# Kernel tuning notes

Measured on AMD Instinct MI355X. Metric: run time of the kernel, lower is better.

## Reference

```python
import jax, jax.numpy as jnp
import numpy as np

D = 1024  # input_size
NORM = 1.0 / np.sqrt(D)


def setup_inputs() -> dict:
    key = jax.random.key(0)
    k_x, k_q, k_k, k_v = jax.random.split(key, 4)
    B, S = 4, 2048
    scale = 1.0 / np.sqrt(D)  # init ~ nn.Linear default magnitude
    return {
        "inputs": jax.random.normal(k_x, (B, S, D), dtype=jnp.float32),
        "Wq": jax.random.uniform(k_q, (D, D), jnp.float32, -scale, scale),
        "Wk": jax.random.uniform(k_k, (D, D), jnp.float32, -scale, scale),
        "Wv": jax.random.uniform(k_v, (D, D), jnp.float32, -scale, scale),
    }


def reference(inputs, Wq, Wk, Wv):
    # nn.Linear(x) = x @ W.T (no bias)
    Q = jnp.einsum("bsd,ed->bse", inputs, Wq)
    K = jnp.einsum("bsd,ed->bse", inputs, Wk)
    V = jnp.einsum("bsd,ed->bse", inputs, Wv)
    attn = jnp.einsum("bqe,bke->bqk", Q, K) * NORM  # [B,S,S]
    attn = jax.nn.softmax(attn, axis=2)
    return jnp.einsum("bqk,bke->bqe", attn, V)
```

## Files before the change

kernel.cpp:

```cpp
#include <hip/hip_runtime.h>

typedef __bf16 bf16_t;
typedef __bf16 bf16x8 __attribute__((ext_vector_type(8)));
typedef __bf16 bf16x4 __attribute__((ext_vector_type(4)));
typedef float  floatx4 __attribute__((ext_vector_type(4)));

__device__ __forceinline__ void gload_lds16(const bf16_t* g, bf16_t* l) {
    __builtin_amdgcn_global_load_lds(
        (const __attribute__((address_space(1))) void*)g,
        (__attribute__((address_space(3))) void*)l,
        16, 0, 0);
}

template <int MODE, int BKT, typename OutT>
__global__ __launch_bounds__(256) void gemm_nt(
    const bf16_t* __restrict__ A, int lda, size_t batchA,
    const bf16_t* __restrict__ B, int ldb, size_t batchB,
    OutT* __restrict__ C, int ldc, size_t batchC,
    bf16_t* __restrict__ C2, int ldc2,
    float* __restrict__ rowsums, int batchR,
    int K, float scale)
{
    constexpr int CH  = BKT / 8;
    constexpr int RPS = 2048 / BKT;
    constexpr int NSHOT = 128 / RPS;

    __shared__ bf16_t sA[128 * BKT];
    __shared__ bf16_t sB[128 * BKT];

    A += (size_t)blockIdx.z * batchA;
    B += (size_t)blockIdx.z * batchB;

    const int tid  = threadIdx.x;
    const int wid  = tid >> 6;
    const int lane = tid & 63;

    const int bm = blockIdx.x * 128;
    const int bn = blockIdx.y * 128;

    const int rr  = tid / CH;
    const int kc8 = (((tid & (CH - 1)) ^ (rr & (CH - 1))) << 3);

    const int wy = (wid >> 1) * 64;
    const int wx = (wid & 1) * 64;
    const int lr = lane & 15;

    floatx4 acc[4][4] = {};

    const bf16_t* pa = A + (size_t)(bm + rr) * lda + kc8;
    const bf16_t* pb = B + (size_t)(bn + rr) * ldb + kc8;
    bf16_t* la = &sA[wid * 512];
    bf16_t* lb = &sB[wid * 512];

    for (int k0 = 0; k0 < K; k0 += BKT) {
        #pragma unroll
        for (int c = 0; c < NSHOT; ++c) {
            gload_lds16(pa + (size_t)(c * RPS) * lda + k0, la + c * 2048);
            gload_lds16(pb + (size_t)(c * RPS) * ldb + k0, lb + c * 2048);
        }
        __syncthreads();

        #pragma unroll
        for (int kk = 0; kk < BKT / 32; ++kk) {
            const int cch = (kk << 2) + (lane >> 4);
            bf16x8 af[4], bq[4];
            #pragma unroll
            for (int i = 0; i < 4; ++i) {
                int r = wy + i * 16 + lr;
                af[i] = *(const bf16x8*)&sA[r * BKT + ((cch ^ (r & (CH - 1))) << 3)];
            }
            #pragma unroll
            for (int j = 0; j < 4; ++j) {
                int r = wx + j * 16 + lr;
                bq[j] = *(const bf16x8*)&sB[r * BKT + ((cch ^ (r & (CH - 1))) << 3)];
            }
            #pragma unroll
            for (int i = 0; i < 4; ++i)
                #pragma unroll
                for (int j = 0; j < 4; ++j)
                    acc[i][j] = __builtin_amdgcn_mfma_f32_16x16x32_bf16(
                        bq[j], af[i], acc[i][j], 0, 0, 0);
        }
        __syncthreads();
    }

    const int cfix = lane & 15;
    const int creg = (lane >> 4) << 2;

    if constexpr (MODE == 1) {
        if (blockIdx.z == 2) {
            #pragma unroll
            for (int i = 0; i < 4; ++i) {
                int mg = bm + wy + i * 16 + cfix;
                #pragma unroll
                for (int j = 0; j < 4; ++j) {
                    int ng = bn + wx + j * 16 + creg;
                    #pragma unroll
                    for (int r = 0; r < 4; ++r)
                        C2[(size_t)(ng + r) * ldc2 + mg] = (bf16_t)acc[i][j][r];
                }
            }
            return;
        }
        OutT* Cz = C + (size_t)blockIdx.z * batchC;
        #pragma unroll
        for (int i = 0; i < 4; ++i) {
            size_t row = (size_t)(bm + wy + i * 16 + cfix);
            #pragma unroll
            for (int j = 0; j < 4; ++j) {
                int col = bn + wx + j * 16 + creg;
                bf16x4 v;
                #pragma unroll
                for (int r = 0; r < 4; ++r) v[r] = (bf16_t)acc[i][j][r];
                *(bf16x4*)&Cz[row * (size_t)ldc + col] = v;
            }
        }
    } else if constexpr (MODE == 2) {
        OutT* Cz = C + (size_t)blockIdx.z * batchC;
        float* sums = rowsums + (size_t)blockIdx.z * batchR;
        float rs[4] = {0.f, 0.f, 0.f, 0.f};
        #pragma unroll
        for (int i = 0; i < 4; ++i) {
            size_t row = (size_t)(bm + wy + i * 16 + cfix);
            #pragma unroll
            for (int j = 0; j < 4; ++j) {
                int col = bn + wx + j * 16 + creg;
                bf16x4 v;
                #pragma unroll
                for (int r = 0; r < 4; ++r) {
                    v[r] = (bf16_t)__expf(acc[i][j][r] * scale);
                    rs[i] += (float)v[r];
                }
                *(bf16x4*)&Cz[row * (size_t)ldc + col] = v;
            }
        }
        #pragma unroll
        for (int i = 0; i < 4; ++i) {
            rs[i] += __shfl_xor(rs[i], 16);
            rs[i] += __shfl_xor(rs[i], 32);
        }
        if (lane < 16) {
            #pragma unroll
            for (int i = 0; i < 4; ++i)
                atomicAdd(&sums[bm + wy + i * 16 + lane], rs[i]);
        }
    } else {
        OutT* Cz = C + (size_t)blockIdx.z * batchC;
        const float* sums = rowsums + (size_t)blockIdx.z * batchR;
        #pragma unroll
        for (int i = 0; i < 4; ++i) {
            int rloc = bm + wy + i * 16 + cfix;
            float rinv = 1.0f / sums[rloc];
            size_t row = (size_t)rloc;
            #pragma unroll
            for (int j = 0; j < 4; ++j) {
                int col = bn + wx + j * 16 + creg;
                floatx4 v;
                #pragma unroll
                for (int r = 0; r < 4; ++r) v[r] = acc[i][j][r] * rinv;
                *(floatx4*)&Cz[row * (size_t)ldc + col] = v;
            }
        }
    }
}

__global__ __launch_bounds__(256) void cvt_all(
    const float* __restrict__ X, const float* __restrict__ Wq,
    const float* __restrict__ Wk, const float* __restrict__ Wv,
    bf16_t* __restrict__ Xb, bf16_t* __restrict__ Wqb,
    bf16_t* __restrict__ Wkb, bf16_t* __restrict__ Wvb,
    float* __restrict__ sums, int nsums,
    int nX4, int nW4)
{
    int i = blockIdx.x * blockDim.x + threadIdx.x;
    if (i < nsums) sums[i] = 0.f;
    const float* src; bf16_t* dst; int idx;
    if (i < nX4) { src = X; dst = Xb; idx = i; }
    else {
        int j = i - nX4;
        int w = j / nW4;
        idx = j - w * nW4;
        if (i >= nX4 + 3 * nW4) return;
        src = (w == 0) ? Wq : (w == 1) ? Wk : Wv;
        dst = (w == 0) ? Wqb : (w == 1) ? Wkb : Wvb;
    }
    float4 v = ((const float4*)src)[idx];
    bf16x4 o;
    o[0] = (bf16_t)v.x; o[1] = (bf16_t)v.y; o[2] = (bf16_t)v.z; o[3] = (bf16_t)v.w;
    *(bf16x4*)(dst + (size_t)idx * 4) = o;
}

extern "C" void kernel_launch(void* const* d_in, const int* in_sizes, int n_in,
                              void* d_out, int out_size, void* d_ws, size_t ws_size,
                              hipStream_t stream)
{
    (void)in_sizes; (void)n_in; (void)out_size; (void)ws_size;
    const float* X  = (const float*)d_in[0];
    const float* Wq = (const float*)d_in[1];
    const float* Wk = (const float*)d_in[2];
    const float* Wv = (const float*)d_in[3];
    float* out = (float*)d_out;

    const int Bb = 4, S = 2048, D = 1024;
    const int M = Bb * S;

    char* ws = (char*)d_ws;
    size_t off = 0;
    auto carve = [&](size_t bytes) -> char* {
        char* p = ws + off;
        off += (bytes + 255) & ~(size_t)255;
        return p;
    };
    bf16_t* Xb  = (bf16_t*)carve((size_t)M * D * 2);
    bf16_t* Wqb = (bf16_t*)carve((size_t)D * D * 2);
    bf16_t* Wkb = (bf16_t*)carve((size_t)D * D * 2);
    bf16_t* Wvb = (bf16_t*)carve((size_t)D * D * 2);
    bf16_t* Qb  = (bf16_t*)carve((size_t)M * D * 2);
    bf16_t* Kb  = (bf16_t*)carve((size_t)M * D * 2);
    bf16_t* Vt  = (bf16_t*)carve((size_t)D * M * 2);
    bf16_t* Sc  = (bf16_t*)carve((size_t)Bb * S * S * 2);
    float*  sums = (float*)carve((size_t)M * 4);

    const int nX4 = M * D / 4, nW4 = D * D / 4;
    const int tot4 = nX4 + 3 * nW4;
    cvt_all<<<(tot4 + 255) / 256, 256, 0, stream>>>(
        X, Wq, Wk, Wv, Xb, Wqb, Wkb, Wvb, sums, M, nX4, nW4);

    gemm_nt<1, 64, bf16_t><<<dim3(M / 128, D / 128, 3), 256, 0, stream>>>(
        Xb, D, 0, Wqb, D, (size_t)D * D, Qb, D, (size_t)M * D,
        Vt, M, nullptr, 0, D, 1.0f);

    gemm_nt<2, 128, bf16_t><<<dim3(S / 128, S / 128, Bb), 256, 0, stream>>>(
        Qb, D, (size_t)S * D, Kb, D, (size_t)S * D, Sc, S, (size_t)S * S,
        nullptr, 0, sums, S, D, 0.03125f);

    gemm_nt<3, 128, float><<<dim3(S / 128, D / 128, Bb), 256, 0, stream>>>(
        Sc, S, (size_t)S * S, Vt, M, (size_t)S, out, D, (size_t)S * D,
        nullptr, 0, sums, S, S, 1.0f);
}
```

Measured before the change: 241.3 us.

## Add 256x256 eight-wave pipelined GEMM for QKV projection and score kernels

```diff
diff --git a/kernel.cpp b/kernel.cpp
--- a/kernel.cpp
+++ b/kernel.cpp
@@ -10,6 +10,174 @@
         (const __attribute__((address_space(1))) void*)g,
         (__attribute__((address_space(3))) void*)l,
         16, 0, 0);
+}
+
+template <int MODE, typename OutT>
+__global__ __launch_bounds__(512, 2) void gemm8p(
+    const bf16_t* __restrict__ A, int lda, size_t batchA,
+    const bf16_t* __restrict__ B, int ldb, size_t batchB,
+    OutT* __restrict__ C, int ldc, size_t batchC,
+    bf16_t* __restrict__ C2, int ldc2,
+    float* __restrict__ rowsums, int batchR,
+    int K, float scale)
+{
+    extern __shared__ __align__(16) bf16_t smem[];
+
+    A += (size_t)blockIdx.z * batchA;
+    B += (size_t)blockIdx.z * batchB;
+
+    const int tid  = threadIdx.x;
+    const int wid  = tid >> 6;
+    const int lane = tid & 63;
+    const int wr   = wid >> 2;
+    const int wc   = wid & 3;
+    const int lr   = lane & 15;
+
+    const int bm = blockIdx.x * 256;
+    const int bn = blockIdx.y * 256;
+
+    const bf16_t* At = A + (size_t)bm * lda;
+    const bf16_t* Bt = B + (size_t)bn * ldb;
+
+    const int    c8 = (((lane & 3) ^ ((lane >> 3) & 3)) << 3);
+    const size_t ga = (size_t)(wid * 16 + (lane >> 2)) * lda + c8;
+    const size_t gb = (size_t)(wid * 16 + (lane >> 2)) * ldb + c8;
+    bf16_t* lw = smem + (wid << 9);
+
+    const int slotoff = (((lane >> 4) ^ ((lr >> 1) & 3)) << 3);
+
+    const int NT = K >> 6;
+
+    floatx4 acc[8][4] = {};
+    bf16x8 af[4], bq[4];
+
+#define STAGE(sbuf, sreg, tile) do {                                          \
+    bf16_t* _l = lw + ((((sbuf) << 2) | (sreg)) << 13);                       \
+    const size_t _k = (size_t)(tile) * 64 + ((sreg) & 1) * 32;                \
+    if ((sreg) >= 2) {                                                        \
+        gload_lds16(Bt + _k + gb, _l);                                        \
+        gload_lds16(Bt + _k + gb + (size_t)128 * ldb, _l + 4096);             \
+    } else {                                                                  \
+        gload_lds16(At + _k + ga, _l);                                        \
+        gload_lds16(At + _k + ga + (size_t)128 * lda, _l + 4096);             \
+    }                                                                         \
+} while (0)
+
+#define LDA_FRAG(buf, kk, row)                                                \
+    (*(const bf16x8*)&smem[((((buf) << 2) | (kk)) << 13) + ((row) << 5) + slotoff])
+#define LDB_FRAG(buf, kk, row)                                                \
+    (*(const bf16x8*)&smem[((((buf) << 2) | (2 + (kk))) << 13) + ((row) << 5) + slotoff])
+
+#define PHASE(buf, kk, mh, RDB, sbuf, sreg, stile, DOVM) do {                 \
+    if (RDB) {                                                                \
+        _Pragma("unroll")                                                     \
+        for (int j = 0; j < 4; ++j)                                           \
+            bq[j] = LDB_FRAG(buf, kk, wc * 64 + j * 16 + lr);                 \
+    }                                                                         \
+    _Pragma("unroll")                                                         \
+    for (int i = 0; i < 4; ++i)                                               \
+        af[i] = LDA_FRAG(buf, kk, wr * 128 + (mh) * 64 + i * 16 + lr);        \
+    STAGE(sbuf, sreg, stile);                                                 \
+    if (DOVM) asm volatile("s_waitcnt vmcnt(6)" ::: "memory");                \
+    __builtin_amdgcn_s_barrier();                                             \
+    __builtin_amdgcn_s_setprio(1);                                            \
+    _Pragma("unroll")                                                         \
+    for (int i = 0; i < 4; ++i) {                                             \
+        _Pragma("unroll")                                                     \
+        for (int j = 0; j < 4; ++j)                                           \
+            acc[(mh) * 4 + i][j] = __builtin_amdgcn_mfma_f32_16x16x32_bf16(   \
+                bq[j], af[i], acc[(mh) * 4 + i][j], 0, 0, 0);                 \
+    }                                                                         \
+    __builtin_amdgcn_s_setprio(0);                                            \
+    __builtin_amdgcn_s_barrier();                                             \
+} while (0)
+
+    STAGE(0, 2, 0); STAGE(0, 0, 0); STAGE(0, 3, 0); STAGE(0, 1, 0);
+    STAGE(1, 2, 1); STAGE(1, 0, 1); STAGE(1, 3, 1);
+    asm volatile("s_waitcnt vmcnt(6)" ::: "memory");
+    __builtin_amdgcn_s_barrier();
+
+    for (int kt = 0; kt < NT; kt += 2) {
+        int t1 = kt + 1;
+        int t2 = kt + 2; if (t2 >= NT) t2 -= NT;
+        int t3 = kt + 3; if (t3 >= NT) t3 -= NT;
+        PHASE(0, 0, 0, true,  1, 1, t1, false);
+        PHASE(0, 0, 1, false, 0, 2, t2, false);
+        PHASE(0, 1, 0, true,  0, 0, t2, false);
+        PHASE(0, 1, 1, false, 0, 3, t2, true);
+        PHASE(1, 0, 0, true,  0, 1, t2, false);
+        PHASE(1, 0, 1, false, 1, 2, t3, false);
+        PHASE(1, 1, 0, true,  1, 0, t3, false);
+        PHASE(1, 1, 1, false, 1, 3, t3, true);
+    }
+    asm volatile("s_waitcnt vmcnt(0)" ::: "memory");
+
+#undef PHASE
+#undef LDA_FRAG
+#undef LDB_FRAG
+#undef STAGE
+
+    const int cfix = lane & 15;
+    const int creg = (lane >> 4) << 2;
+
+    if constexpr (MODE == 1) {
+        if (blockIdx.z == 2) {
+            #pragma unroll
+            for (int mi = 0; mi < 8; ++mi) {
+                int mg = bm + wr * 128 + mi * 16 + cfix;
+                #pragma unroll
+                for (int j = 0; j < 4; ++j) {
+                    int ng = bn + wc * 64 + j * 16 + creg;
+                    #pragma unroll
+                    for (int r = 0; r < 4; ++r)
+                        C2[(size_t)(ng + r) * ldc2 + mg] = (bf16_t)acc[mi][j][r];
+                }
+            }
+            return;
+        }
+        OutT* Cz = C + (size_t)blockIdx.z * batchC;
+        #pragma unroll
+        for (int mi = 0; mi < 8; ++mi) {
+            size_t row = (size_t)(bm + wr * 128 + mi * 16 + cfix);
+            #pragma unroll
+            for (int j = 0; j < 4; ++j) {
+                int col = bn + wc * 64 + j * 16 + creg;
+                bf16x4 v;
+                #pragma unroll
+                for (int r = 0; r < 4; ++r) v[r] = (bf16_t)acc[mi][j][r];
+                *(bf16x4*)&Cz[row * (size_t)ldc + col] = v;
+            }
+        }
+    } else {
+        OutT* Cz = C + (size_t)blockIdx.z * batchC;
+        float* sums = rowsums + (size_t)blockIdx.z * batchR;
+        float rs[8] = {};
+        #pragma unroll
+        for (int mi = 0; mi < 8; ++mi) {
+            size_t row = (size_t)(bm + wr * 128 + mi * 16 + cfix);
+            #pragma unroll
+            for (int j = 0; j < 4; ++j) {
+                int col = bn + wc * 64 + j * 16 + creg;
+                bf16x4 v;
+                #pragma unroll
+                for (int r = 0; r < 4; ++r) {
+                    v[r] = (bf16_t)__expf(acc[mi][j][r] * scale);
+                    rs[mi] += (float)v[r];
+                }
+                *(bf16x4*)&Cz[row * (size_t)ldc + col] = v;
+            }
+        }
+        #pragma unroll
+        for (int mi = 0; mi < 8; ++mi) {
+            rs[mi] += __shfl_xor(rs[mi], 16);
+            rs[mi] += __shfl_xor(rs[mi], 32);
+        }
+        if (lane < 16) {
+            #pragma unroll
+            for (int mi = 0; mi < 8; ++mi)
+                atomicAdd(&sums[bm + wr * 128 + mi * 16 + lane], rs[mi]);
+        }
+    }
 }
 
 template <int MODE, int BKT, typename OutT>
@@ -63,7 +231,7 @@
         #pragma unroll
         for (int kk = 0; kk < BKT / 32; ++kk) {
             const int cch = (kk << 2) + (lane >> 4);
-            bf16x8 af[4], bq[4];
+            bf16x8 af[4], bqf[4];
             #pragma unroll
             for (int i = 0; i < 4; ++i) {
                 int r = wy + i * 16 + lr;
@@ -72,14 +240,14 @@
             #pragma unroll
             for (int j = 0; j < 4; ++j) {
                 int r = wx + j * 16 + lr;
-                bq[j] = *(const bf16x8*)&sB[r * BKT + ((cch ^ (r & (CH - 1))) << 3)];
+                bqf[j] = *(const bf16x8*)&sB[r * BKT + ((cch ^ (r & (CH - 1))) << 3)];
             }
             #pragma unroll
             for (int i = 0; i < 4; ++i)
                 #pragma unroll
                 for (int j = 0; j < 4; ++j)
                     acc[i][j] = __builtin_amdgcn_mfma_f32_16x16x32_bf16(
-                        bq[j], af[i], acc[i][j], 0, 0, 0);
+                        bqf[j], af[i], acc[i][j], 0, 0, 0);
         }
         __syncthreads();
     }
@@ -87,64 +255,7 @@
     const int cfix = lane & 15;
     const int creg = (lane >> 4) << 2;
 
-    if constexpr (MODE == 1) {
-        if (blockIdx.z == 2) {
-            #pragma unroll
-            for (int i = 0; i < 4; ++i) {
-                int mg = bm + wy + i * 16 + cfix;
-                #pragma unroll
-                for (int j = 0; j < 4; ++j) {
-                    int ng = bn + wx + j * 16 + creg;
-                    #pragma unroll
-                    for (int r = 0; r < 4; ++r)
-                        C2[(size_t)(ng + r) * ldc2 + mg] = (bf16_t)acc[i][j][r];
-                }
-            }
-            return;
-        }
-        OutT* Cz = C + (size_t)blockIdx.z * batchC;
-        #pragma unroll
-        for (int i = 0; i < 4; ++i) {
-            size_t row = (size_t)(bm + wy + i * 16 + cfix);
-            #pragma unroll
-            for (int j = 0; j < 4; ++j) {
-                int col = bn + wx + j * 16 + creg;
-                bf16x4 v;
-                #pragma unroll
-                for (int r = 0; r < 4; ++r) v[r] = (bf16_t)acc[i][j][r];
-                *(bf16x4*)&Cz[row * (size_t)ldc + col] = v;
-            }
-        }
-    } else if constexpr (MODE == 2) {
-        OutT* Cz = C + (size_t)blockIdx.z * batchC;
-        float* sums = rowsums + (size_t)blockIdx.z * batchR;
-        float rs[4] = {0.f, 0.f, 0.f, 0.f};
-        #pragma unroll
-        for (int i = 0; i < 4; ++i) {
-            size_t row = (size_t)(bm + wy + i * 16 + cfix);
-            #pragma unroll
-            for (int j = 0; j < 4; ++j) {
-                int col = bn + wx + j * 16 + creg;
-                bf16x4 v;
-                #pragma unroll
-                for (int r = 0; r < 4; ++r) {
-                    v[r] = (bf16_t)__expf(acc[i][j][r] * scale);
-                    rs[i] += (float)v[r];
-                }
-                *(bf16x4*)&Cz[row * (size_t)ldc + col] = v;
-            }
-        }
-        #pragma unroll
-        for (int i = 0; i < 4; ++i) {
-            rs[i] += __shfl_xor(rs[i], 16);
-            rs[i] += __shfl_xor(rs[i], 32);
-        }
-        if (lane < 16) {
-            #pragma unroll
-            for (int i = 0; i < 4; ++i)
-                atomicAdd(&sums[bm + wy + i * 16 + lane], rs[i]);
-        }
-    } else {
+    if constexpr (MODE == 3) {
         OutT* Cz = C + (size_t)blockIdx.z * batchC;
         const float* sums = rowsums + (size_t)blockIdx.z * batchR;
         #pragma unroll
@@ -162,6 +273,7 @@
             }
         }
     }
+    (void)C2; (void)ldc2; (void)scale;
 }
 
 __global__ __launch_bounds__(256) void cvt_all(
@@ -221,16 +333,27 @@
     bf16_t* Sc  = (bf16_t*)carve((size_t)Bb * S * S * 2);
     float*  sums = (float*)carve((size_t)M * 4);
 
+    static bool s_attr = false;
+    if (!s_attr) {
+        (void)hipFuncSetAttribute(
+            reinterpret_cast<const void*>(&gemm8p<1, bf16_t>),
+            hipFuncAttributeMaxDynamicSharedMemorySize, 131072);
+        (void)hipFuncSetAttribute(
+            reinterpret_cast<const void*>(&gemm8p<2, bf16_t>),
+            hipFuncAttributeMaxDynamicSharedMemorySize, 131072);
+        s_attr = true;
+    }
+
     const int nX4 = M * D / 4, nW4 = D * D / 4;
     const int tot4 = nX4 + 3 * nW4;
     cvt_all<<<(tot4 + 255) / 256, 256, 0, stream>>>(
         X, Wq, Wk, Wv, Xb, Wqb, Wkb, Wvb, sums, M, nX4, nW4);
 
-    gemm_nt<1, 64, bf16_t><<<dim3(M / 128, D / 128, 3), 256, 0, stream>>>(
+    gemm8p<1, bf16_t><<<dim3(M / 256, D / 256, 3), 512, 131072, stream>>>(
         Xb, D, 0, Wqb, D, (size_t)D * D, Qb, D, (size_t)M * D,
         Vt, M, nullptr, 0, D, 1.0f);
 
-    gemm_nt<2, 128, bf16_t><<<dim3(S / 128, S / 128, Bb), 256, 0, stream>>>(
+    gemm8p<2, bf16_t><<<dim3(S / 256, S / 256, Bb), 512, 131072, stream>>>(
         Qb, D, (size_t)S * D, Kb, D, (size_t)S * D, Sc, S, (size_t)S * S,
         nullptr, 0, sums, S, D, 0.03125f);
 
```

Result: faster. 234.5 us (-2.8%).
